# Kernel optimization log

Hardware: AMD Instinct MI355X
Metric: run time of the kernel (lower is better)

The kernel has to match this reference:

```python
import jax, jax.numpy as jnp
import numpy as np

DIM = 1024
N_HEADS = 16
HEAD_DIM = DIM // N_HEADS


def setup_inputs() -> dict:
    key = jax.random.key(0)
    k_x, k_qkv, k_out = jax.random.split(key, 3)
    B, L = 4, 2048
    x = jax.random.normal(k_x, (B, L, DIM), dtype=jnp.float32)
    # torch Linear weight has shape [out, in]; y = x @ W.T
    s = 1.0 / np.sqrt(DIM)
    W_qkv = jax.random.uniform(k_qkv, (3 * DIM, DIM), dtype=jnp.float32, minval=-s, maxval=s)
    W_out = jax.random.uniform(k_out, (DIM, DIM), dtype=jnp.float32, minval=-s, maxval=s)
    return {"x": x, "W_qkv": W_qkv, "W_out": W_out}


def reference(x, W_qkv, W_out):
    B, L, D = x.shape
    H, Hd = N_HEADS, HEAD_DIM
    scale = Hd ** (-0.5)
    qkv = x @ W_qkv.T                       # [B, L, 3D]
    q, k, v = jnp.split(qkv, 3, axis=-1)
    # 'b l (h d) -> b h l d'
    q = q.reshape(B, L, H, Hd).transpose(0, 2, 1, 3)
    k = k.reshape(B, L, H, Hd).transpose(0, 2, 1, 3)
    v = v.reshape(B, L, H, Hd).transpose(0, 2, 1, 3)
    attn = jnp.einsum('bhld,bhmd->bhlm', q, k) * scale  # [B, H, L, L]
    causal = jnp.tril(jnp.ones((L, L), dtype=bool))
    attn = jnp.where(causal, attn, -jnp.inf)
    attn = jax.nn.softmax(attn, axis=-1)
    out = jnp.einsum('bhlm,bhmd->bhld', attn, v)        # [B, H, L, Hd]
    out = out.transpose(0, 2, 1, 3).reshape(B, L, D)    # 'b h l d -> b l (h d)'
    return out @ W_out.T
```

## Files before the change

### kernel.cpp

```cpp
#include <hip/hip_runtime.h>
#include <stdint.h>

#define BATCH 4
#define SEQ   2048
#define DIM_  1024
#define NHEAD 16
#define HDIM  64

#define QSC 0.18033688011112042f

typedef __attribute__((ext_vector_type(8)))  short bf8;
typedef __attribute__((ext_vector_type(4)))  short s4v;
typedef __attribute__((ext_vector_type(4)))  float f4;
typedef __attribute__((ext_vector_type(16))) float f16v;

#define MFMA(a, b, c)   __builtin_amdgcn_mfma_f32_16x16x32_bf16(a, b, c, 0, 0, 0)
#define MFMA32(a, b, c) __builtin_amdgcn_mfma_f32_32x32x16_bf16(a, b, c, 0, 0, 0)

#define BAR_LGKM() asm volatile("s_waitcnt lgkmcnt(0)\n\ts_barrier" ::: "memory")

static __device__ __forceinline__ short f2b(float f) {
    uint32_t u = __builtin_bit_cast(uint32_t, f);
    u = (u + 0x7FFFu + ((u >> 16) & 1u)) >> 16;
    return (short)u;
}

typedef const uint32_t __attribute__((address_space(1)))* gas_t;
typedef uint32_t __attribute__((address_space(3)))* las_t;
static __device__ __forceinline__ void gl_lds16(const short* g, short* l) {
    __builtin_amdgcn_global_load_lds((gas_t)g, (las_t)l, 16, 0, 0);
}

__global__ void cvt_f32_bf16(const float* __restrict__ in, short* __restrict__ out, int n4) {
    int i = blockIdx.x * blockDim.x + threadIdx.x;
    if (i < n4) {
        float4 v = ((const float4*)in)[i];
        s4v o;
        o.x = f2b(v.x); o.y = f2b(v.y); o.z = f2b(v.z); o.w = f2b(v.w);
        ((s4v*)out)[i] = o;
    }
}

__global__ __launch_bounds__(256) void gemm_qkv(const short* __restrict__ A,
                                                const short* __restrict__ W,
                                                short* __restrict__ Qd,
                                                short* __restrict__ Kd,
                                                short* __restrict__ Vd,
                                                int M, int N, int K) {
    __shared__ __align__(16) short As[128 * 32];
    __shared__ __align__(16) short Bs[128 * 32];

    const int tid  = threadIdx.x;
    const int lane = tid & 63;
    const int wave = tid >> 6;
    const int quad = lane >> 4, l16 = lane & 15;
    const int wr = wave >> 1, wc = wave & 1;
    const int m0 = blockIdx.y * 128;
    const int n0 = blockIdx.x * 128;

    const int srow   = tid >> 2;
    const int schunk = (tid & 3) * 8;
    const short* Ag0 = A + (size_t)(m0 + srow) * K + schunk;
    const short* Ag1 = Ag0 + (size_t)64 * K;
    const short* Bg0 = W + (size_t)(n0 + srow) * K + schunk;
    const short* Bg1 = Bg0 + (size_t)64 * K;
    short* Al0 = As + srow * 32 + schunk;
    short* Al1 = Al0 + 64 * 32;
    short* Bl0 = Bs + srow * 32 + schunk;
    short* Bl1 = Bl0 + 64 * 32;

    const short* afp = As + (wr * 64 + l16) * 32 + quad * 8;
    const short* bfp = Bs + (wc * 64 + l16) * 32 + quad * 8;

    f4 acc[4][4] = {};

    for (int k0 = 0; k0 < K; k0 += 32) {
        __syncthreads();
        gl_lds16(Ag0 + k0, Al0);
        gl_lds16(Ag1 + k0, Al1);
        gl_lds16(Bg0 + k0, Bl0);
        gl_lds16(Bg1 + k0, Bl1);
        __syncthreads();

        bf8 a[4], b[4];
        #pragma unroll
        for (int i = 0; i < 4; ++i) {
            a[i] = *(const bf8*)(afp + i * 16 * 32);
            b[i] = *(const bf8*)(bfp + i * 16 * 32);
        }
        #pragma unroll
        for (int mt = 0; mt < 4; ++mt)
            #pragma unroll
            for (int nt = 0; nt < 4; ++nt)
                acc[mt][nt] = MFMA(a[mt], b[nt], acc[mt][nt]);
    }

    short* const bases[3] = {Qd, Kd, Vd};
    #pragma unroll
    for (int mt = 0; mt < 4; ++mt) {
        const int row = m0 + wr * 64 + mt * 16 + quad * 4;
        #pragma unroll
        for (int nt = 0; nt < 4; ++nt) {
            const int colb  = n0 + wc * 64 + nt * 16;
            const int which = colb >> 10;
            const int hh    = (colb >> 6) & 15;
            const int d0    = colb & 63;
            const float sc_ = (which == 0) ? QSC : 1.0f;
            short* bp = bases[which];
            #pragma unroll
            for (int r = 0; r < 4; ++r) {
                const int t  = row + r;
                const int bb = t >> 11, ll = t & 2047;
                bp[((size_t)(bb * NHEAD + hh) * SEQ + ll) * 64 + d0 + l16] =
                    f2b(acc[mt][nt][r] * sc_);
            }
        }
    }
}

__global__ __launch_bounds__(256) void gemm_bt(const short* __restrict__ A,
                                               const short* __restrict__ W,
                                               float* __restrict__ Cp,
                                               int M, int N, int K) {
    __shared__ __align__(16) short As[128 * 32];
    __shared__ __align__(16) short Bs[128 * 32];

    const int tid  = threadIdx.x;
    const int lane = tid & 63;
    const int wave = tid >> 6;
    const int quad = lane >> 4, l16 = lane & 15;
    const int wr = wave >> 1, wc = wave & 1;
    const int m0 = blockIdx.y * 128;
    const int n0 = blockIdx.x * 128;

    const int srow   = tid >> 2;
    const int schunk = (tid & 3) * 8;
    const short* Ag0 = A + (size_t)(m0 + srow) * K + schunk;
    const short* Ag1 = Ag0 + (size_t)64 * K;
    const short* Bg0 = W + (size_t)(n0 + srow) * K + schunk;
    const short* Bg1 = Bg0 + (size_t)64 * K;
    short* Al0 = As + srow * 32 + schunk;
    short* Al1 = Al0 + 64 * 32;
    short* Bl0 = Bs + srow * 32 + schunk;
    short* Bl1 = Bl0 + 64 * 32;

    const short* afp = As + (wr * 64 + l16) * 32 + quad * 8;
    const short* bfp = Bs + (wc * 64 + l16) * 32 + quad * 8;

    f4 acc[4][4] = {};

    for (int k0 = 0; k0 < K; k0 += 32) {
        __syncthreads();
        gl_lds16(Ag0 + k0, Al0);
        gl_lds16(Ag1 + k0, Al1);
        gl_lds16(Bg0 + k0, Bl0);
        gl_lds16(Bg1 + k0, Bl1);
        __syncthreads();

        bf8 a[4], b[4];
        #pragma unroll
        for (int i = 0; i < 4; ++i) {
            a[i] = *(const bf8*)(afp + i * 16 * 32);
            b[i] = *(const bf8*)(bfp + i * 16 * 32);
        }
        #pragma unroll
        for (int mt = 0; mt < 4; ++mt)
            #pragma unroll
            for (int nt = 0; nt < 4; ++nt)
                acc[mt][nt] = MFMA(a[mt], b[nt], acc[mt][nt]);
    }

    #pragma unroll
    for (int mt = 0; mt < 4; ++mt) {
        const int row = m0 + wr * 64 + mt * 16 + quad * 4;
        #pragma unroll
        for (int nt = 0; nt < 4; ++nt) {
            const int col = n0 + wc * 64 + nt * 16 + l16;
            #pragma unroll
            for (int r = 0; r < 4; ++r)
                Cp[(size_t)(row + r) * N + col] = acc[mt][nt][r];
        }
    }
}

__global__ __launch_bounds__(256) void flash_attn(const short* __restrict__ Qd,
                                                  const short* __restrict__ Kd,
                                                  const short* __restrict__ Vd,
                                                  short* __restrict__ out) {
    const int bh = blockIdx.x;
    const int b  = bh >> 4, h = bh & 15;
    const int qt = (gridDim.y - 1) - blockIdx.y;
    const int q0 = qt * 128;
    const int tid  = threadIdx.x;
    const int lane = tid & 63, wave = tid >> 6;
    const int l32  = lane & 31, khalf = lane >> 5;

    __shared__ __align__(16) short Ks[64 * 72];
    __shared__ __align__(16) short Vt[64 * 72];
    uint32_t* Vt32 = (uint32_t*)Vt;

    const short* Qp = Qd + (size_t)bh * (SEQ * 64);
    const short* Kp = Kd + (size_t)bh * (SEQ * 64);
    const short* Vp = Vd + (size_t)bh * (SEQ * 64);

    const int qrow = q0 + wave * 32 + l32;
    bf8 qf[4];
    #pragma unroll
    for (int dk = 0; dk < 4; ++dk)
        qf[dk] = *(const bf8*)(Qp + (size_t)qrow * 64 + dk * 16 + khalf * 8);

    const int skey = tid >> 2, sc = tid & 3;
    const int vkp = tid & 31, vds = (tid >> 5) * 8;

    bf8 ka0 = *(const bf8*)(Kp + (size_t)skey * 64 + sc * 8);
    bf8 ka1 = *(const bf8*)(Kp + (size_t)skey * 64 + (sc + 4) * 8);
    bf8 vr0 = *(const bf8*)(Vp + (size_t)(2 * vkp) * 64 + vds);
    bf8 vr1 = *(const bf8*)(Vp + (size_t)(2 * vkp + 1) * 64 + vds);

    f16v o0 = {}, o1 = {};
    float lsum = 0.f;
    const bf8 zz = {};

    const int nIter = 2 * qt + 2;
    for (int it = 0; it < nIter; ++it) {
        const int k0 = it * 64;

        BAR_LGKM();
        *(bf8*)(&Ks[skey * 72 + sc * 8])       = ka0;
        *(bf8*)(&Ks[skey * 72 + (sc + 4) * 8]) = ka1;
        #pragma unroll
        for (int i = 0; i < 8; ++i) {
            uint32_t p = (uint32_t)(uint16_t)vr0[i] | ((uint32_t)(uint16_t)vr1[i] << 16);
            Vt32[(vds + i) * 36 + vkp] = p;
        }
        BAR_LGKM();

        if (it + 1 < nIter) {
            const int kn = k0 + 64;
            ka0 = *(const bf8*)(Kp + (size_t)(kn + skey) * 64 + sc * 8);
            ka1 = *(const bf8*)(Kp + (size_t)(kn + skey) * 64 + (sc + 4) * 8);
            vr0 = *(const bf8*)(Vp + (size_t)(kn + 2 * vkp) * 64 + vds);
            vr1 = *(const bf8*)(Vp + (size_t)(kn + 2 * vkp + 1) * 64 + vds);
        }

        bf8 pf[4];
        #pragma unroll
        for (int kt = 0; kt < 2; ++kt) {
            const int ktbase = k0 + kt * 32;
            const int rel = (q0 + wave * 32) - ktbase;
            if (rel < 0) {
                pf[kt * 2] = zz; pf[kt * 2 + 1] = zz;
                continue;
            }
            f16v st = {};
            #pragma unroll
            for (int dk = 0; dk < 4; ++dk) {
                bf8 kf = *(const bf8*)(&Ks[(kt * 32 + l32) * 72 + dk * 16 + khalf * 8]);
                st = MFMA32(kf, qf[dk], st);
            }
            float P[16];
            if (rel == 0) {
                #pragma unroll
                for (int r = 0; r < 16; ++r) {
                    const int kg = ktbase + (r & 3) + 8 * (r >> 2) + 4 * khalf;
                    float pv = __builtin_amdgcn_exp2f(st[r]);
                    P[r] = (kg > qrow) ? 0.0f : pv;
                }
            } else {
                #pragma unroll
                for (int r = 0; r < 16; ++r) P[r] = __builtin_amdgcn_exp2f(st[r]);
            }
            float e0[4], e1[4];
            #pragma unroll
            for (int j = 0; j < 4; ++j) {
                e0[j] = __shfl_xor(khalf ? P[j] : P[4 + j], 32);
                e1[j] = __shfl_xor(khalf ? P[8 + j] : P[12 + j], 32);
            }
            bf8 f0, f1;
            float ls = 0.f;
            #pragma unroll
            for (int j = 0; j < 4; ++j) {
                const float a0 = khalf ? e0[j] : P[j];
                const float b0 = khalf ? P[4 + j] : e0[j];
                const float a1 = khalf ? e1[j] : P[8 + j];
                const float b1 = khalf ? P[12 + j] : e1[j];
                f0[j] = f2b(a0); f0[4 + j] = f2b(b0);
                f1[j] = f2b(a1); f1[4 + j] = f2b(b1);
                ls += a0 + b0 + a1 + b1;
            }
            lsum += ls;
            pf[kt * 2]     = f0;
            pf[kt * 2 + 1] = f1;
        }

        #pragma unroll
        for (int ks = 0; ks < 4; ++ks) {
            bf8 v0 = *(const bf8*)(&Vt[(l32) * 72 + ks * 16 + khalf * 8]);
            bf8 v1 = *(const bf8*)(&Vt[(32 + l32) * 72 + ks * 16 + khalf * 8]);
            o0 = MFMA32(pf[ks], v0, o0);
            o1 = MFMA32(pf[ks], v1, o1);
        }
    }

    lsum += __shfl_xor(lsum, 32);
    short* outp = out + ((size_t)(b * SEQ + q0 + wave * 32) * DIM_) + h * 64;
    #pragma unroll
    for (int r = 0; r < 16; ++r) {
        const int rowl = (r & 3) + 8 * (r >> 2) + 4 * khalf;
        const float inv = 1.0f / __shfl(lsum, rowl);
        outp[(size_t)rowl * DIM_ + l32]      = f2b(o0[r] * inv);
        outp[(size_t)rowl * DIM_ + 32 + l32] = f2b(o1[r] * inv);
    }
}

extern "C" void kernel_launch(void* const* d_in, const int* in_sizes, int n_in,
                              void* d_out, int out_size, void* d_ws, size_t ws_size,
                              hipStream_t stream) {
    const float* x    = (const float*)d_in[0];
    const float* wqkv = (const float*)d_in[1];
    const float* wout = (const float*)d_in[2];

    char* ws = (char*)d_ws;
    short* xb    = (short*)(ws);
    short* wqkvb = (short*)(ws + (size_t)(16) * (1 << 20));
    short* woutb = (short*)(ws + (size_t)(22) * (1 << 20));
    short* Qd    = (short*)(ws + (size_t)(24) * (1 << 20));
    short* Kd    = (short*)(ws + (size_t)(40) * (1 << 20));
    short* Vd    = (short*)(ws + (size_t)(56) * (1 << 20));
    short* attnb = (short*)(ws + (size_t)(72) * (1 << 20));

    int n4;
    n4 = BATCH * SEQ * DIM_ / 4;
    cvt_f32_bf16<<<(n4 + 255) / 256, 256, 0, stream>>>(x, xb, n4);
    n4 = 3 * DIM_ * DIM_ / 4;
    cvt_f32_bf16<<<(n4 + 255) / 256, 256, 0, stream>>>(wqkv, wqkvb, n4);
    n4 = DIM_ * DIM_ / 4;
    cvt_f32_bf16<<<(n4 + 255) / 256, 256, 0, stream>>>(wout, woutb, n4);

    gemm_qkv<<<dim3(3 * DIM_ / 128, BATCH * SEQ / 128), 256, 0, stream>>>(
        xb, wqkvb, Qd, Kd, Vd, BATCH * SEQ, 3 * DIM_, DIM_);

    flash_attn<<<dim3(BATCH * NHEAD, SEQ / 128), 256, 0, stream>>>(Qd, Kd, Vd, attnb);

    gemm_bt<<<dim3(DIM_ / 128, BATCH * SEQ / 128), 256, 0, stream>>>(
        attnb, woutb, (float*)d_out, BATCH * SEQ, DIM_, DIM_);
}
```

Measured before the change: 265.7 us.

## Swizzle GEMM LDS layout, merge conversion kernels, skip fully masked attention waves

Merges the three fp32-to-bf16 conversion launches into a single kernel. Applies an XOR swizzle to the GEMM LDS tile layout, matched on the fragment reads, to reduce bank conflicts, and hardcodes K=1024 into shared prologue and loop macros. In flash attention, a wave whose query rows all lie before the current key block now skips its compute after the shared loads and barriers. The swizzle must line up exactly with the global_load_lds lane mapping, and the early continue must stay clear of any later barrier in the loop.

```diff
diff --git a/kernel.cpp b/kernel.cpp
--- a/kernel.cpp
+++ b/kernel.cpp
@@ -31,69 +31,71 @@
     __builtin_amdgcn_global_load_lds((gas_t)g, (las_t)l, 16, 0, 0);
 }
 
-__global__ void cvt_f32_bf16(const float* __restrict__ in, short* __restrict__ out, int n4) {
+__global__ void cvt_all(const float* __restrict__ x, const float* __restrict__ wq,
+                        const float* __restrict__ wo, short* __restrict__ xb,
+                        short* __restrict__ wqb, short* __restrict__ wob) {
+    const int NX = BATCH * SEQ * DIM_ / 4, NQ = 3 * DIM_ * DIM_ / 4;
     int i = blockIdx.x * blockDim.x + threadIdx.x;
-    if (i < n4) {
-        float4 v = ((const float4*)in)[i];
-        s4v o;
-        o.x = f2b(v.x); o.y = f2b(v.y); o.z = f2b(v.z); o.w = f2b(v.w);
-        ((s4v*)out)[i] = o;
-    }
-}
+    const float4* in; s4v* out; int j;
+    if (i < NX)           { in = (const float4*)x;  out = (s4v*)xb;  j = i; }
+    else if (i < NX + NQ) { in = (const float4*)wq; out = (s4v*)wqb; j = i - NX; }
+    else                  { in = (const float4*)wo; out = (s4v*)wob; j = i - NX - NQ; }
+    float4 v = in[j];
+    s4v o;
+    o.x = f2b(v.x); o.y = f2b(v.y); o.z = f2b(v.z); o.w = f2b(v.w);
+    out[j] = o;
+}
+
+#define GEMM_PROLOG()                                                         \
+    __shared__ __align__(16) short As[128 * 32];                              \
+    __shared__ __align__(16) short Bs[128 * 32];                              \
+    const int tid  = threadIdx.x;                                             \
+    const int lane = tid & 63;                                                \
+    const int wave = tid >> 6;                                                \
+    const int quad = lane >> 4, l16 = lane & 15;                              \
+    const int wr = wave >> 1, wc = wave & 1;                                  \
+    const int m0 = blockIdx.y * 128;                                          \
+    const int n0 = blockIdx.x * 128;                                          \
+    const int srow = tid >> 2;                                                \
+    const int sx   = ((tid & 3) ^ ((tid >> 3) & 3)) * 8;    \
+    const short* Ag0 = A + (size_t)(m0 + srow) * 1024 + sx;                   \
+    const short* Ag1 = Ag0 + (size_t)64 * 1024;                               \
+    const short* Bg0 = W + (size_t)(n0 + srow) * 1024 + sx;                   \
+    const short* Bg1 = Bg0 + (size_t)64 * 1024;                               \
+    short* Al0 = As + tid * 8;                     \
+    short* Al1 = Al0 + 64 * 32;                                               \
+    short* Bl0 = Bs + tid * 8;                                                \
+    short* Bl1 = Bl0 + 64 * 32;                                               \
+    const int akey = (l16 >> 1) & 3;                                          \
+    const short* afp = As + (wr * 64 + l16) * 32 + (quad ^ akey) * 8;         \
+    const short* bfp = Bs + (wc * 64 + l16) * 32 + (quad ^ akey) * 8;         \
+    f4 acc[4][4] = {};
+
+#define GEMM_KLOOP()                                                          \
+    for (int k0 = 0; k0 < 1024; k0 += 32) {                                   \
+        __syncthreads();                                                      \
+        gl_lds16(Ag0 + k0, Al0);                                              \
+        gl_lds16(Ag1 + k0, Al1);                                              \
+        gl_lds16(Bg0 + k0, Bl0);                                              \
+        gl_lds16(Bg1 + k0, Bl1);                                              \
+        __syncthreads();                                                      \
+        bf8 a[4], b[4];                                                       \
+        _Pragma("unroll") for (int i = 0; i < 4; ++i) {                       \
+            a[i] = *(const bf8*)(afp + i * 16 * 32);                          \
+            b[i] = *(const bf8*)(bfp + i * 16 * 32);                          \
+        }                                                                     \
+        _Pragma("unroll") for (int mt = 0; mt < 4; ++mt)                      \
+            _Pragma("unroll") for (int nt = 0; nt < 4; ++nt)                  \
+                acc[mt][nt] = MFMA(a[mt], b[nt], acc[mt][nt]);                \
+    }
 
 __global__ __launch_bounds__(256) void gemm_qkv(const short* __restrict__ A,
                                                 const short* __restrict__ W,
                                                 short* __restrict__ Qd,
                                                 short* __restrict__ Kd,
-                                                short* __restrict__ Vd,
-                                                int M, int N, int K) {
-    __shared__ __align__(16) short As[128 * 32];
-    __shared__ __align__(16) short Bs[128 * 32];
-
-    const int tid  = threadIdx.x;
-    const int lane = tid & 63;
-    const int wave = tid >> 6;
-    const int quad = lane >> 4, l16 = lane & 15;
-    const int wr = wave >> 1, wc = wave & 1;
-    const int m0 = blockIdx.y * 128;
-    const int n0 = blockIdx.x * 128;
-
-    const int srow   = tid >> 2;
-    const int schunk = (tid & 3) * 8;
-    const short* Ag0 = A + (size_t)(m0 + srow) * K + schunk;
-    const short* Ag1 = Ag0 + (size_t)64 * K;
-    const short* Bg0 = W + (size_t)(n0 + srow) * K + schunk;
-    const short* Bg1 = Bg0 + (size_t)64 * K;
-    short* Al0 = As + srow * 32 + schunk;
-    short* Al1 = Al0 + 64 * 32;
-    short* Bl0 = Bs + srow * 32 + schunk;
-    short* Bl1 = Bl0 + 64 * 32;
-
-    const short* afp = As + (wr * 64 + l16) * 32 + quad * 8;
-    const short* bfp = Bs + (wc * 64 + l16) * 32 + quad * 8;
-
-    f4 acc[4][4] = {};
-
-    for (int k0 = 0; k0 < K; k0 += 32) {
-        __syncthreads();
-        gl_lds16(Ag0 + k0, Al0);
-        gl_lds16(Ag1 + k0, Al1);
-        gl_lds16(Bg0 + k0, Bl0);
-        gl_lds16(Bg1 + k0, Bl1);
-        __syncthreads();
-
-        bf8 a[4], b[4];
-        #pragma unroll
-        for (int i = 0; i < 4; ++i) {
-            a[i] = *(const bf8*)(afp + i * 16 * 32);
-            b[i] = *(const bf8*)(bfp + i * 16 * 32);
-        }
-        #pragma unroll
-        for (int mt = 0; mt < 4; ++mt)
-            #pragma unroll
-            for (int nt = 0; nt < 4; ++nt)
-                acc[mt][nt] = MFMA(a[mt], b[nt], acc[mt][nt]);
-    }
+                                                short* __restrict__ Vd) {
+    GEMM_PROLOG();
+    GEMM_KLOOP();
 
     short* const bases[3] = {Qd, Kd, Vd};
     #pragma unroll
@@ -120,55 +122,9 @@
 
 __global__ __launch_bounds__(256) void gemm_bt(const short* __restrict__ A,
                                                const short* __restrict__ W,
-                                               float* __restrict__ Cp,
-                                               int M, int N, int K) {
-    __shared__ __align__(16) short As[128 * 32];
-    __shared__ __align__(16) short Bs[128 * 32];
-
-    const int tid  = threadIdx.x;
-    const int lane = tid & 63;
-    const int wave = tid >> 6;
-    const int quad = lane >> 4, l16 = lane & 15;
-    const int wr = wave >> 1, wc = wave & 1;
-    const int m0 = blockIdx.y * 128;
-    const int n0 = blockIdx.x * 128;
-
-    const int srow   = tid >> 2;
-    const int schunk = (tid & 3) * 8;
-    const short* Ag0 = A + (size_t)(m0 + srow) * K + schunk;
-    const short* Ag1 = Ag0 + (size_t)64 * K;
-    const short* Bg0 = W + (size_t)(n0 + srow) * K + schunk;
-    const short* Bg1 = Bg0 + (size_t)64 * K;
-    short* Al0 = As + srow * 32 + schunk;
-    short* Al1 = Al0 + 64 * 32;
-    short* Bl0 = Bs + srow * 32 + schunk;
-    short* Bl1 = Bl0 + 64 * 32;
-
-    const short* afp = As + (wr * 64 + l16) * 32 + quad * 8;
-    const short* bfp = Bs + (wc * 64 + l16) * 32 + quad * 8;
-
-    f4 acc[4][4] = {};
-
-    for (int k0 = 0; k0 < K; k0 += 32) {
-        __syncthreads();
-        gl_lds16(Ag0 + k0, Al0);
-        gl_lds16(Ag1 + k0, Al1);
-        gl_lds16(Bg0 + k0, Bl0);
-        gl_lds16(Bg1 + k0, Bl1);
-        __syncthreads();
-
-        bf8 a[4], b[4];
-        #pragma unroll
-        for (int i = 0; i < 4; ++i) {
-            a[i] = *(const bf8*)(afp + i * 16 * 32);
-            b[i] = *(const bf8*)(bfp + i * 16 * 32);
-        }
-        #pragma unroll
-        for (int mt = 0; mt < 4; ++mt)
-            #pragma unroll
-            for (int nt = 0; nt < 4; ++nt)
-                acc[mt][nt] = MFMA(a[mt], b[nt], acc[mt][nt]);
-    }
+                                               float* __restrict__ Cp) {
+    GEMM_PROLOG();
+    GEMM_KLOOP();
 
     #pragma unroll
     for (int mt = 0; mt < 4; ++mt) {
@@ -178,7 +134,7 @@
             const int col = n0 + wc * 64 + nt * 16 + l16;
             #pragma unroll
             for (int r = 0; r < 4; ++r)
-                Cp[(size_t)(row + r) * N + col] = acc[mt][nt][r];
+                Cp[(size_t)(row + r) * DIM_ + col] = acc[mt][nt][r];
         }
     }
 }
@@ -243,6 +199,8 @@
             vr1 = *(const bf8*)(Vp + (size_t)(kn + 2 * vkp + 1) * 64 + vds);
         }
 
+        if (q0 + wave * 32 < k0) continue;
+
         bf8 pf[4];
         #pragma unroll
         for (int kt = 0; kt < 2; ++kt) {
@@ -329,19 +287,14 @@
     short* Vd    = (short*)(ws + (size_t)(56) * (1 << 20));
     short* attnb = (short*)(ws + (size_t)(72) * (1 << 20));
 
-    int n4;
-    n4 = BATCH * SEQ * DIM_ / 4;
-    cvt_f32_bf16<<<(n4 + 255) / 256, 256, 0, stream>>>(x, xb, n4);
-    n4 = 3 * DIM_ * DIM_ / 4;
-    cvt_f32_bf16<<<(n4 + 255) / 256, 256, 0, stream>>>(wqkv, wqkvb, n4);
-    n4 = DIM_ * DIM_ / 4;
-    cvt_f32_bf16<<<(n4 + 255) / 256, 256, 0, stream>>>(wout, woutb, n4);
+    const int ntot = (BATCH * SEQ * DIM_ + 3 * DIM_ * DIM_ + DIM_ * DIM_) / 4;
+    cvt_all<<<(ntot + 255) / 256, 256, 0, stream>>>(x, wqkv, wout, xb, wqkvb, woutb);
 
     gemm_qkv<<<dim3(3 * DIM_ / 128, BATCH * SEQ / 128), 256, 0, stream>>>(
-        xb, wqkvb, Qd, Kd, Vd, BATCH * SEQ, 3 * DIM_, DIM_);
+        xb, wqkvb, Qd, Kd, Vd);
 
     flash_attn<<<dim3(BATCH * NHEAD, SEQ / 128), 256, 0, stream>>>(Qd, Kd, Vd, attnb);
 
     gemm_bt<<<dim3(DIM_ / 128, BATCH * SEQ / 128), 256, 0, stream>>>(
-        attnb, woutb, (float*)d_out, BATCH * SEQ, DIM_, DIM_);
-}
+        attnb, woutb, (float*)d_out);
+}
```

Measured after the change: 248.4 us. -6.5%, faster.
